# Performance work log

Measured on AMD Instinct MI355X. Metric: run time of the kernel, lower is better.

The kernel has to match this reference:

```python
import jax, jax.numpy as jnp
import numpy as np
from jax import lax

SIGMA = 1.0
TRUNCATE = 4.0  # skimage.filters.gaussian default


def _gauss_kernel(sigma, truncate=TRUNCATE):
    radius = int(truncate * sigma + 0.5)
    t = np.arange(-radius, radius + 1, dtype=np.float32)
    k = np.exp(-0.5 * (t / sigma) ** 2)
    k = k / k.sum()
    return jnp.asarray(k), radius


def setup_inputs() -> dict:
    key = jax.random.key(0)
    x = jax.random.uniform(key, (128, 1, 512, 512), dtype=jnp.float32)
    return {"x": x}


def _blur(x, sigma=SIGMA):
    # x: [B, 1, H, W] -> squeeze channel like the torch module, blur, return [B, H, W]
    k, r = _gauss_kernel(sigma)
    K = 2 * r + 1
    # 'nearest' boundary mode of skimage == edge padding
    xp = jnp.pad(x, ((0, 0), (0, 0), (r, r), (r, r)), mode="edge")
    kh = k.reshape(1, 1, K, 1).astype(x.dtype)  # vertical pass
    kw = k.reshape(1, 1, 1, K).astype(x.dtype)  # horizontal pass
    dn = lax.conv_dimension_numbers(xp.shape, kh.shape, ("NCHW", "OIHW", "NCHW"))
    y = lax.conv_general_dilated(xp, kh, (1, 1), "VALID", dimension_numbers=dn)
    y = lax.conv_general_dilated(y, kw, (1, 1), "VALID", dimension_numbers=dn)
    return y[:, 0]  # [B, H, W], matching x_i.squeeze() per-sample output


def reference(x):
    return _blur(x)
```

## Files before the change

### kernel.cpp

```cpp
#include <hip/hip_runtime.h>

namespace {

constexpr int R     = 4;
constexpr int TSX   = 64;
constexpr int TSY   = 32;
constexpr int HSX   = TSX + 2*R;
constexpr int HSY   = TSY + 2*R;
constexpr int VSTR  = 76;
constexpr int NVX   = HSX / 4;
constexpr int IMG_H = 512;
constexpr int IMG_W = 512;

__device__ __forceinline__ int clampi(int v, int lo, int hi) {
    return v < lo ? lo : (v > hi ? hi : v);
}

__global__ __launch_bounds__(256)
void gauss_blur_kernel(const float* __restrict__ in, float* __restrict__ out) {
    const float KW[9] = {
        1.3383062e-4f, 4.4318616e-3f, 5.3990966e-2f, 2.4197144e-1f,
        3.9894347e-1f, 2.4197144e-1f, 5.3990966e-2f, 4.4318616e-3f,
        1.3383062e-4f};

    __shared__ float s_in[HSY * VSTR];
    __shared__ float s_v [TSY * VSTR];

    const int tid = threadIdx.x;
    const int b   = blockIdx.z;
    const int ty0 = blockIdx.y * TSY;
    const int tx0 = blockIdx.x * TSX;

    const float* __restrict__ inb = in + (size_t)b * IMG_H * IMG_W;

    for (int i = tid; i < HSY * NVX; i += 256) {
        int ly = i / NVX;
        int v  = i - ly * NVX;
        int gy = clampi(ty0 + ly - R, 0, IMG_H - 1);
        int gx = tx0 - R + 4 * v;
        const float* rp = inb + gy * IMG_W;
        float4 val;
        if (gx >= 0 && gx <= IMG_W - 4) {
            val = *reinterpret_cast<const float4*>(rp + gx);
        } else {
            val.x = rp[clampi(gx + 0, 0, IMG_W - 1)];
            val.y = rp[clampi(gx + 1, 0, IMG_W - 1)];
            val.z = rp[clampi(gx + 2, 0, IMG_W - 1)];
            val.w = rp[clampi(gx + 3, 0, IMG_W - 1)];
        }
        *reinterpret_cast<float4*>(&s_in[ly * VSTR + 4 * v]) = val;
    }
    __syncthreads();

    for (int i = tid; i < TSY * NVX; i += 256) {
        int ly = i / NVX;
        int v  = i - ly * NVX;
        float4 acc = {0.f, 0.f, 0.f, 0.f};
        #pragma unroll
        for (int t = 0; t < 9; ++t) {
            float4 a = *reinterpret_cast<const float4*>(&s_in[(ly + t) * VSTR + 4 * v]);
            acc.x = fmaf(KW[t], a.x, acc.x);
            acc.y = fmaf(KW[t], a.y, acc.y);
            acc.z = fmaf(KW[t], a.z, acc.z);
            acc.w = fmaf(KW[t], a.w, acc.w);
        }
        *reinterpret_cast<float4*>(&s_v[ly * VSTR + 4 * v]) = acc;
    }
    __syncthreads();

    float* __restrict__ outb = out + (size_t)b * IMG_H * IMG_W;
    for (int i = tid; i < TSY * (TSX / 4); i += 256) {
        int ly = i >> 4;
        int j  = i & 15;
        const float* vp = &s_v[ly * VSTR + 4 * j];
        float4 a = *reinterpret_cast<const float4*>(vp);
        float4 bq = *reinterpret_cast<const float4*>(vp + 4);
        float4 c = *reinterpret_cast<const float4*>(vp + 8);
        float w[12] = {a.x, a.y, a.z, a.w, bq.x, bq.y, bq.z, bq.w, c.x, c.y, c.z, c.w};
        float4 o;
        float acc0 = 0.f, acc1 = 0.f, acc2 = 0.f, acc3 = 0.f;
        #pragma unroll
        for (int t = 0; t < 9; ++t) {
            acc0 = fmaf(KW[t], w[t + 0], acc0);
            acc1 = fmaf(KW[t], w[t + 1], acc1);
            acc2 = fmaf(KW[t], w[t + 2], acc2);
            acc3 = fmaf(KW[t], w[t + 3], acc3);
        }
        o.x = acc0; o.y = acc1; o.z = acc2; o.w = acc3;
        *reinterpret_cast<float4*>(&outb[(ty0 + ly) * IMG_W + tx0 + 4 * j]) = o;
    }
}

}

extern "C" void kernel_launch(void* const* d_in, const int* in_sizes, int n_in,
                              void* d_out, int out_size, void* d_ws, size_t ws_size,
                              hipStream_t stream) {
    const float* x = (const float*)d_in[0];
    float* out = (float*)d_out;

    const int batch = in_sizes[0] / (IMG_H * IMG_W);

    dim3 grid(IMG_W / TSX, IMG_H / TSY, batch);
    gauss_blur_kernel<<<grid, 256, 0, stream>>>(x, out);
}
```

Measured before the change: 62.12 us.

## Do horizontal pass from global loads, vertical pass with register blocking

Reorders the separable blur so the horizontal pass runs directly on global float4 loads and writes into a single shared buffer, then the vertical pass computes four output rows per thread using register accumulators and stores straight to global memory. The tile grows to 64x64, which reduces vertical halo overhead, and one shared buffer and one barrier are removed. Overlapping global loads (three float4 per thread for the horizontal halo) rely on the caches, and occupancy is set through the launch bounds hint.

Result: slower. 107.7 us (+73.4%).

```diff
diff --git a/kernel.cpp b/kernel.cpp
--- a/kernel.cpp
+++ b/kernel.cpp
@@ -4,11 +4,9 @@
 
 constexpr int R     = 4;
 constexpr int TSX   = 64;
-constexpr int TSY   = 32;
-constexpr int HSX   = TSX + 2*R;
-constexpr int HSY   = TSY + 2*R;
-constexpr int VSTR  = 76;
-constexpr int NVX   = HSX / 4;
+constexpr int TSY   = 64;
+constexpr int HR    = TSY + 2 * R;
+constexpr int HSTR  = TSX + 4;
 constexpr int IMG_H = 512;
 constexpr int IMG_W = 512;
 
@@ -16,15 +14,14 @@
     return v < lo ? lo : (v > hi ? hi : v);
 }
 
-__global__ __launch_bounds__(256)
+__global__ __launch_bounds__(256, 8)
 void gauss_blur_kernel(const float* __restrict__ in, float* __restrict__ out) {
     const float KW[9] = {
         1.3383062e-4f, 4.4318616e-3f, 5.3990966e-2f, 2.4197144e-1f,
         3.9894347e-1f, 2.4197144e-1f, 5.3990966e-2f, 4.4318616e-3f,
         1.3383062e-4f};
 
-    __shared__ float s_in[HSY * VSTR];
-    __shared__ float s_v [TSY * VSTR];
+    __shared__ float hbuf[HR * HSTR];
 
     const int tid = threadIdx.x;
     const int b   = blockIdx.z;
@@ -33,61 +30,68 @@
 
     const float* __restrict__ inb = in + (size_t)b * IMG_H * IMG_W;
 
-    for (int i = tid; i < HSY * NVX; i += 256) {
-        int ly = i / NVX;
-        int v  = i - ly * NVX;
-        int gy = clampi(ty0 + ly - R, 0, IMG_H - 1);
-        int gx = tx0 - R + 4 * v;
+    for (int i = tid; i < HR * (TSX / 4); i += 256) {
+        int r  = i >> 4;
+        int j  = i & 15;
+        int gy = clampi(ty0 - R + r, 0, IMG_H - 1);
         const float* rp = inb + gy * IMG_W;
-        float4 val;
-        if (gx >= 0 && gx <= IMG_W - 4) {
-            val = *reinterpret_cast<const float4*>(rp + gx);
-        } else {
-            val.x = rp[clampi(gx + 0, 0, IMG_W - 1)];
-            val.y = rp[clampi(gx + 1, 0, IMG_W - 1)];
-            val.z = rp[clampi(gx + 2, 0, IMG_W - 1)];
-            val.w = rp[clampi(gx + 3, 0, IMG_W - 1)];
+        int xo = tx0 + 4 * j;
+
+        float w[12];
+        #pragma unroll
+        for (int v = 0; v < 3; ++v) {
+            int a = xo - 4 + 4 * v;
+            float4 val;
+            if (a >= 0 && a <= IMG_W - 4) {
+                val = *reinterpret_cast<const float4*>(rp + a);
+            } else {
+                val.x = rp[clampi(a + 0, 0, IMG_W - 1)];
+                val.y = rp[clampi(a + 1, 0, IMG_W - 1)];
+                val.z = rp[clampi(a + 2, 0, IMG_W - 1)];
+                val.w = rp[clampi(a + 3, 0, IMG_W - 1)];
+            }
+            w[4 * v + 0] = val.x; w[4 * v + 1] = val.y;
+            w[4 * v + 2] = val.z; w[4 * v + 3] = val.w;
         }
-        *reinterpret_cast<float4*>(&s_in[ly * VSTR + 4 * v]) = val;
+
+        float a0 = 0.f, a1 = 0.f, a2 = 0.f, a3 = 0.f;
+        #pragma unroll
+        for (int t = 0; t < 9; ++t) {
+            a0 = fmaf(KW[t], w[t + 0], a0);
+            a1 = fmaf(KW[t], w[t + 1], a1);
+            a2 = fmaf(KW[t], w[t + 2], a2);
+            a3 = fmaf(KW[t], w[t + 3], a3);
+        }
+        float4 o = {a0, a1, a2, a3};
+        *reinterpret_cast<float4*>(&hbuf[r * HSTR + 4 * j]) = o;
     }
     __syncthreads();
 
-    for (int i = tid; i < TSY * NVX; i += 256) {
-        int ly = i / NVX;
-        int v  = i - ly * NVX;
-        float4 acc = {0.f, 0.f, 0.f, 0.f};
+    const int px  = tid & 15;
+    const int py  = tid >> 4;
+    const int lx  = 4 * px;
+    const int oy0 = 4 * py;
+
+    float4 acc[4] = {{0,0,0,0},{0,0,0,0},{0,0,0,0},{0,0,0,0}};
+    #pragma unroll
+    for (int t = 0; t < 12; ++t) {
+        float4 h = *reinterpret_cast<const float4*>(&hbuf[(oy0 + t) * HSTR + lx]);
         #pragma unroll
-        for (int t = 0; t < 9; ++t) {
-            float4 a = *reinterpret_cast<const float4*>(&s_in[(ly + t) * VSTR + 4 * v]);
-            acc.x = fmaf(KW[t], a.x, acc.x);
-            acc.y = fmaf(KW[t], a.y, acc.y);
-            acc.z = fmaf(KW[t], a.z, acc.z);
-            acc.w = fmaf(KW[t], a.w, acc.w);
+        for (int rr = 0; rr < 4; ++rr) {
+            int k = t - rr;
+            if (k >= 0 && k < 9) {
+                acc[rr].x = fmaf(KW[k], h.x, acc[rr].x);
+                acc[rr].y = fmaf(KW[k], h.y, acc[rr].y);
+                acc[rr].z = fmaf(KW[k], h.z, acc[rr].z);
+                acc[rr].w = fmaf(KW[k], h.w, acc[rr].w);
+            }
         }
-        *reinterpret_cast<float4*>(&s_v[ly * VSTR + 4 * v]) = acc;
     }
-    __syncthreads();
 
     float* __restrict__ outb = out + (size_t)b * IMG_H * IMG_W;
-    for (int i = tid; i < TSY * (TSX / 4); i += 256) {
-        int ly = i >> 4;
-        int j  = i & 15;
-        const float* vp = &s_v[ly * VSTR + 4 * j];
-        float4 a = *reinterpret_cast<const float4*>(vp);
-        float4 bq = *reinterpret_cast<const float4*>(vp + 4);
-        float4 c = *reinterpret_cast<const float4*>(vp + 8);
-        float w[12] = {a.x, a.y, a.z, a.w, bq.x, bq.y, bq.z, bq.w, c.x, c.y, c.z, c.w};
-        float4 o;
-        float acc0 = 0.f, acc1 = 0.f, acc2 = 0.f, acc3 = 0.f;
-        #pragma unroll
-        for (int t = 0; t < 9; ++t) {
-            acc0 = fmaf(KW[t], w[t + 0], acc0);
-            acc1 = fmaf(KW[t], w[t + 1], acc1);
-            acc2 = fmaf(KW[t], w[t + 2], acc2);
-            acc3 = fmaf(KW[t], w[t + 3], acc3);
-        }
-        o.x = acc0; o.y = acc1; o.z = acc2; o.w = acc3;
-        *reinterpret_cast<float4*>(&outb[(ty0 + ly) * IMG_W + tx0 + 4 * j]) = o;
+    #pragma unroll
+    for (int rr = 0; rr < 4; ++rr) {
+        *reinterpret_cast<float4*>(&outb[(ty0 + oy0 + rr) * IMG_W + tx0 + lx]) = acc[rr];
     }
 }
 
```
